# Performance work log

Hardware: AMD Instinct MI355X
Metric: run time of the kernel (lower is better)

## Reference

```python
import jax, jax.numpy as jnp
import numpy as np
from jax import lax

B, C, O, K, H, Wd = 8, 64, 64, 3, 128, 128


def setup_inputs() -> dict:
    key = jax.random.key(0)
    k1, k2, k3 = jax.random.split(key, 3)
    feat = jax.random.normal(k1, (B, C, H, Wd), dtype=jnp.float32)
    transform_mat = jax.random.normal(k2, (B, K * K, H * Wd), dtype=jnp.float32)
    # xavier-normal init for W [C, K, K, O]
    std = float(np.sqrt(2.0 / (C * K * K + O)))
    W = jax.random.normal(k3, (C, K, K, O), dtype=jnp.float32) * std
    return {"feat": feat, "transform_mat": transform_mat, "W": W}


def reference(feat, transform_mat, W):
    b, c, h, w = feat.shape
    L = h * w
    # unfold: [B, C*K*K, H, W] with channel-major (c, ki, kj) ordering, same as torch Unfold
    patches = lax.conv_general_dilated_patches(
        feat, filter_shape=(K, K), window_strides=(1, 1),
        padding=((1, 1), (1, 1)))
    p = patches.reshape(b, c, K * K, L)                 # [B, C, K*K, L]
    trans = jnp.transpose(transform_mat, (0, 2, 1))     # [B, L, K*K] (module's permute(0,2,1))
    Wr = W.reshape(c, K * K, -1)                        # [C, K*K, O]
    # dynamic weighted conv: per-location filter scales each patch tap before contraction
    out = jnp.einsum('bckl,blk,cko->bol', p, trans, Wr)  # [B, O, L]
    return out.reshape(b, -1, h, w)
```

## Files before the change

### kernel.cpp

```cpp
#include <hip/hip_runtime.h>

#define NTAP 9
#define C_DIM 64
#define O_DIM 64
#define HW 128

typedef short s16x8 __attribute__((ext_vector_type(8)));
typedef float f32x16 __attribute__((ext_vector_type(16)));

__device__ __forceinline__ unsigned short f2bf(float x) {
    unsigned int u = __float_as_uint(x);
    unsigned int r = (u + 0x7fffu + ((u >> 16) & 1u)) >> 16;
    return (unsigned short)r;
}

__global__ void swizzle_W_kernel(const float* __restrict__ W,
                                 unsigned short* __restrict__ Wf) {
    int idx = blockIdx.x * 256 + threadIdx.x;
    if (idx >= NTAP * 4 * 2 * 64 * 8) return;
    int e    = idx & 7;
    int lane = (idx >> 3) & 63;
    int m    = (idx >> 9) & 1;
    int s    = (idx >> 10) & 3;
    int tap  = idx >> 12;
    int c = s * 16 + ((lane >> 5) << 3) + e;
    int o = (m << 5) + (lane & 31);
    Wf[idx] = f2bf(W[c * 576 + tap * 64 + o]);
}

__global__ __launch_bounds__(512, 4) void dyconv_kernel(
    const float* __restrict__ feat, const float* __restrict__ tm,
    const unsigned short* __restrict__ Wf, float* __restrict__ out)
{
    __shared__ __align__(16) unsigned short feat_lds[4][66][64];

    const int flat  = blockIdx.x;
    const int b     = flat & 7;
    const int inner = flat >> 3;
    const int h0    = (inner >> 1) * 2;
    const int w0    = (inner & 1) << 6;

    const int tid  = threadIdx.x;
    const int lane = tid & 63;
    const int wave = tid >> 6;
    const int hrow = (wave >> 2) & 1;
    const int m    = (wave >> 1) & 1;
    const int pg   = wave & 1;
    const int g    = lane >> 5;
    const int c31  = lane & 31;
    const int pw   = pg * 32 + c31;
    const int wout = w0 + pw;
    const int hout = h0 + hrow;

    auto do_unit = [&](int U) {
        const int oct = U & 7;
        const int t6  = U >> 3;
        const int q   = t6 % 18;
        const int r   = t6 / 18;
        const int hr  = h0 - 1 + r;
        const int wb  = w0 - 4 + 4 * q;
        const bool ld = (hr >= 0) && (hr < HW) && (wb >= 0) && (wb <= HW - 4);
        const float* src = feat + (((size_t)(b * C_DIM + oct * 8)) * HW + hr) * HW + wb;
        float4 v[8];
        #pragma unroll
        for (int j = 0; j < 8; ++j)
            v[j] = ld ? *(const float4*)(src + (size_t)j * (HW * HW))
                      : float4{0.f, 0.f, 0.f, 0.f};
        #pragma unroll
        for (int i = 0; i < 4; ++i) {
            const int wi = 4 * q - 3 + i;
            if (wi >= 0 && wi <= 65) {
                const int slot = oct ^ (wi & 7);
                s16x8 pk;
                #pragma unroll
                for (int j = 0; j < 8; ++j) {
                    const float* vf = (const float*)&v[j];
                    pk[j] = (short)f2bf(vf[i]);
                }
                *(s16x8*)&feat_lds[r][wi][slot * 8] = pk;
            }
        }
    };

    float tmr[NTAP];
    #pragma unroll
    for (int t = 0; t < NTAP; ++t)
        tmr[t] = tm[((size_t)(b * NTAP + t)) * (HW * HW) + (size_t)hout * HW + wout];

    do_unit(tid);
    if ((tid & 7) == 0) do_unit(512 + (tid >> 3));

    __syncthreads();

    const s16x8* __restrict__ Wf8 = (const s16x8*)Wf;

    f32x16 acc = {0,0,0,0,0,0,0,0,0,0,0,0,0,0,0,0};

    __builtin_amdgcn_s_setprio(1);
    #pragma unroll
    for (int tap = 0; tap < NTAP; ++tap) {
        const int di = tap / 3;
        const int dj = tap % 3;
        const int wi = pw + dj;
        const int sw = wi & 7;
        f32x16 pa = {0,0,0,0,0,0,0,0,0,0,0,0,0,0,0,0};
        #pragma unroll
        for (int s = 0; s < 4; ++s) {
            const int slot = (2 * s + g) ^ sw;
            s16x8 bf = *(const s16x8*)&feat_lds[hrow + di][wi][slot * 8];
            s16x8 a  = Wf8[((tap * 4 + s) * 2 + m) * 64 + lane];
            pa = __builtin_amdgcn_mfma_f32_32x32x16_bf16(a, bf, pa, 0, 0, 0);
        }
        const float tv = tmr[tap];
        #pragma unroll
        for (int r = 0; r < 16; ++r)
            acc[r] = fmaf(tv, pa[r], acc[r]);
    }
    __builtin_amdgcn_s_setprio(0);

    float* op = out + ((size_t)b * O_DIM) * (HW * HW) + (size_t)hout * HW + wout;
    #pragma unroll
    for (int r = 0; r < 16; ++r) {
        const int o = (r & 3) + ((r >> 2) << 3) + (g << 2) + (m << 5);
        op[(size_t)o * (HW * HW)] = acc[r];
    }
}

extern "C" void kernel_launch(void* const* d_in, const int* in_sizes, int n_in,
                              void* d_out, int out_size, void* d_ws, size_t ws_size,
                              hipStream_t stream) {
    const float* feat = (const float*)d_in[0];
    const float* tm   = (const float*)d_in[1];
    const float* W    = (const float*)d_in[2];
    float* out        = (float*)d_out;
    unsigned short* Wf = (unsigned short*)d_ws;

    swizzle_W_kernel<<<dim3(144), dim3(256), 0, stream>>>(W, Wf);
    dyconv_kernel<<<dim3(1024), dim3(512), 0, stream>>>(feat, tm, Wf, out);
}
```

Measured before the change: 38.49 us.

## Shrink conv tiles to one row by 32 columns and use packed bf16 conversion

Each block now covers one output row of 32 pixels with 2 waves (128 threads), launched as 4096 blocks instead of 1024 blocks of 512 threads that covered 2x64 tiles. The LDS halo tile drops from 4x66 to 3x34 positions, and the bf16 packing now uses the v_cvt_pk_bf16_f32 instruction instead of manual rounding. Smaller blocks should spread work more evenly and cut LDS use per block. The cost is a larger halo overhead per output, since 3 rows are loaded for 1 output row, so each feature element is read from global memory more often.

```diff
diff --git a/kernel.cpp b/kernel.cpp
--- a/kernel.cpp
+++ b/kernel.cpp
@@ -14,6 +14,12 @@
     return (unsigned short)r;
 }
 
+__device__ __forceinline__ unsigned int cvt_pk_bf16(float lo, float hi) {
+    unsigned int r;
+    asm("v_cvt_pk_bf16_f32 %0, %1, %2" : "=v"(r) : "v"(lo), "v"(hi));
+    return r;
+}
+
 __global__ void swizzle_W_kernel(const float* __restrict__ W,
                                  unsigned short* __restrict__ Wf) {
     int idx = blockIdx.x * 256 + threadIdx.x;
@@ -28,36 +34,31 @@
     Wf[idx] = f2bf(W[c * 576 + tap * 64 + o]);
 }
 
-__global__ __launch_bounds__(512, 4) void dyconv_kernel(
+__global__ __launch_bounds__(128, 6) void dyconv_kernel(
     const float* __restrict__ feat, const float* __restrict__ tm,
     const unsigned short* __restrict__ Wf, float* __restrict__ out)
 {
-    __shared__ __align__(16) unsigned short feat_lds[4][66][64];
+    __shared__ __align__(16) unsigned short feat_lds[3][34][64];
 
     const int flat  = blockIdx.x;
     const int b     = flat & 7;
     const int inner = flat >> 3;
-    const int h0    = (inner >> 1) * 2;
-    const int w0    = (inner & 1) << 6;
+    const int h     = inner >> 2;
+    const int w0    = (inner & 3) << 5;
 
     const int tid  = threadIdx.x;
     const int lane = tid & 63;
-    const int wave = tid >> 6;
-    const int hrow = (wave >> 2) & 1;
-    const int m    = (wave >> 1) & 1;
-    const int pg   = wave & 1;
+    const int m    = tid >> 6;
     const int g    = lane >> 5;
     const int c31  = lane & 31;
-    const int pw   = pg * 32 + c31;
-    const int wout = w0 + pw;
-    const int hout = h0 + hrow;
+    const int wout = w0 + c31;
 
     auto do_unit = [&](int U) {
         const int oct = U & 7;
-        const int t6  = U >> 3;
-        const int q   = t6 % 18;
-        const int r   = t6 / 18;
-        const int hr  = h0 - 1 + r;
+        const int t3  = U >> 3;
+        const int q   = t3 % 10;
+        const int r   = t3 / 10;
+        const int hr  = h - 1 + r;
         const int wb  = w0 - 4 + 4 * q;
         const bool ld = (hr >= 0) && (hr < HW) && (wb >= 0) && (wb <= HW - 4);
         const float* src = feat + (((size_t)(b * C_DIM + oct * 8)) * HW + hr) * HW + wb;
@@ -69,15 +70,14 @@
         #pragma unroll
         for (int i = 0; i < 4; ++i) {
             const int wi = 4 * q - 3 + i;
-            if (wi >= 0 && wi <= 65) {
+            if (wi >= 0 && wi <= 33) {
                 const int slot = oct ^ (wi & 7);
-                s16x8 pk;
-                #pragma unroll
-                for (int j = 0; j < 8; ++j) {
-                    const float* vf = (const float*)&v[j];
-                    pk[j] = (short)f2bf(vf[i]);
-                }
-                *(s16x8*)&feat_lds[r][wi][slot * 8] = pk;
+                int4 pk;
+                pk.x = cvt_pk_bf16(((const float*)&v[0])[i], ((const float*)&v[1])[i]);
+                pk.y = cvt_pk_bf16(((const float*)&v[2])[i], ((const float*)&v[3])[i]);
+                pk.z = cvt_pk_bf16(((const float*)&v[4])[i], ((const float*)&v[5])[i]);
+                pk.w = cvt_pk_bf16(((const float*)&v[6])[i], ((const float*)&v[7])[i]);
+                *(int4*)&feat_lds[r][wi][slot * 8] = pk;
             }
         }
     };
@@ -85,14 +85,14 @@
     float tmr[NTAP];
     #pragma unroll
     for (int t = 0; t < NTAP; ++t)
-        tmr[t] = tm[((size_t)(b * NTAP + t)) * (HW * HW) + (size_t)hout * HW + wout];
+        tmr[t] = tm[((size_t)(b * NTAP + t)) * (HW * HW) + (size_t)h * HW + wout];
 
     do_unit(tid);
-    if ((tid & 7) == 0) do_unit(512 + (tid >> 3));
+    if (tid < 112) do_unit(tid + 128);
 
     __syncthreads();
 
-    const s16x8* __restrict__ Wf8 = (const s16x8*)Wf;
+    const s16x8* __restrict__ wbase = (const s16x8*)Wf + (size_t)m * 64 + lane;
 
     f32x16 acc = {0,0,0,0,0,0,0,0,0,0,0,0,0,0,0,0};
 
@@ -101,14 +101,14 @@
     for (int tap = 0; tap < NTAP; ++tap) {
         const int di = tap / 3;
         const int dj = tap % 3;
-        const int wi = pw + dj;
+        const int wi = c31 + dj;
         const int sw = wi & 7;
         f32x16 pa = {0,0,0,0,0,0,0,0,0,0,0,0,0,0,0,0};
         #pragma unroll
         for (int s = 0; s < 4; ++s) {
             const int slot = (2 * s + g) ^ sw;
-            s16x8 bf = *(const s16x8*)&feat_lds[hrow + di][wi][slot * 8];
-            s16x8 a  = Wf8[((tap * 4 + s) * 2 + m) * 64 + lane];
+            s16x8 bf = *(const s16x8*)&feat_lds[di][wi][slot * 8];
+            s16x8 a  = wbase[(tap * 4 + s) * 128];
             pa = __builtin_amdgcn_mfma_f32_32x32x16_bf16(a, bf, pa, 0, 0, 0);
         }
         const float tv = tmr[tap];
@@ -118,7 +118,7 @@
     }
     __builtin_amdgcn_s_setprio(0);
 
-    float* op = out + ((size_t)b * O_DIM) * (HW * HW) + (size_t)hout * HW + wout;
+    float* op = out + ((size_t)b * O_DIM) * (HW * HW) + (size_t)h * HW + wout;
     #pragma unroll
     for (int r = 0; r < 16; ++r) {
         const int o = (r & 3) + ((r >> 2) << 3) + (g << 2) + (m << 5);
@@ -136,5 +136,5 @@
     unsigned short* Wf = (unsigned short*)d_ws;
 
     swizzle_W_kernel<<<dim3(144), dim3(256), 0, stream>>>(W, Wf);
-    dyconv_kernel<<<dim3(1024), dim3(512), 0, stream>>>(feat, tm, Wf, out);
+    dyconv_kernel<<<dim3(4096), dim3(128), 0, stream>>>(feat, tm, Wf, out);
 }
```

Result: slower. 42.56 us (+10.6%).
